# Kernel optimization log

Hardware: AMD Instinct MI355X
Metric: run time of the kernel (lower is better)

Reference implementation:

```python
import jax, jax.numpy as jnp
import numpy as np

B, T = 16384, 79
DIMS = [(1, 64), (64, 32), (32, 16), (16, 8), (8, 16), (16, 32), (32, 64), (64, 79)]


def _simple_rnn(x, Wx, Wh, b, act, return_seq):
    # x: [B, T, D] -> SimpleRNN: h_t = act(x_t @ Wx + h_{t-1} @ Wh + b)
    xb = jnp.einsum('btd,du->btu', x, Wx) + b  # precompute input projection
    h0 = jnp.zeros((x.shape[0], Wh.shape[0]), x.dtype)

    def step(h, xt):
        h = act(xt + h @ Wh)
        return h, h

    hT, hs = jax.lax.scan(step, h0, jnp.swapaxes(xb, 0, 1))  # scan over time
    return jnp.swapaxes(hs, 0, 1) if return_seq else hT


def setup_inputs() -> dict:
    key = jax.random.key(0)
    ks = jax.random.split(key, 3 * len(DIMS) + 1)
    inp = {"x": jax.random.normal(ks[0], (B, T), dtype=jnp.float32)}
    for i, (d, u) in enumerate(DIMS):
        inp[f"Wx{i}"] = jax.random.normal(ks[1 + 3 * i], (d, u), dtype=jnp.float32) / np.sqrt(d).astype(np.float32)
        inp[f"Wh{i}"] = jax.random.normal(ks[2 + 3 * i], (u, u), dtype=jnp.float32) / np.sqrt(u).astype(np.float32)
        inp[f"b{i}"] = jnp.zeros((u,), dtype=jnp.float32)
    return inp


def reference(x, Wx0, Wh0, b0, Wx1, Wh1, b1, Wx2, Wh2, b2, Wx3, Wh3, b3,
              Wx4, Wh4, b4, Wx5, Wh5, b5, Wx6, Wh6, b6, Wx7, Wh7, b7):
    params = [(Wx0, Wh0, b0), (Wx1, Wh1, b1), (Wx2, Wh2, b2), (Wx3, Wh3, b3),
              (Wx4, Wh4, b4), (Wx5, Wh5, b5), (Wx6, Wh6, b6), (Wx7, Wh7, b7)]
    h = x[..., None]  # [B, T, 1]  (tf.expand_dims(x, -1))
    n = len(params)
    for i, (Wx, Wh, b) in enumerate(params):
        last = i == n - 1
        act = jax.nn.sigmoid if last else jax.nn.relu
        h = _simple_rnn(h, Wx, Wh, b, act, return_seq=not last)
    return h  # decoded: [B, 79]
```

## Files before the change

kernel.cpp:

```cpp
#include <hip/hip_runtime.h>
#include <hip/hip_bf16.h>

#define DEVFN static __device__ __forceinline__

typedef short bf16x8 __attribute__((ext_vector_type(8)));
typedef float f32x4  __attribute__((ext_vector_type(4)));

constexpr int TSEQ  = 79;
constexpr int MWG   = 16;
constexpr int ROWU  = 344;
constexpr int NBLK  = 16384 / 64;

constexpr int LD[8]   = {1,64,32,16,8,16,32,64};
constexpr int LU[8]   = {64,32,16,8,16,32,64,79};
constexpr int LS[8]   = {0,8,72,104,120,128,144,176};
constexpr int LO[8]   = {8,72,104,120,128,144,176,240};
constexpr int LKP[8]  = {96,96,64,32,32,64,96,160};
constexpr int LKS[8]  = {3,3,2,1,1,2,3,5};
constexpr int LUP[8]  = {64,32,16,16,16,32,64,80};
constexpr int WOFF[8] = {0,6144,9216,10240,10752,11264,13312,19456};
constexpr int WTOTAL  = 32256;

constexpr int NT[8]  = {4,2,1,1,1,2,4,5};
constexpr int AO[8]  = {0,12,18,20,21,22,26,38};
constexpr int TO[8]  = {0,4,6,7,8,9,11,15};
constexpr int NH[8]  = {3,1,1,0,0,1,2,3};
constexpr int BHO[8] = {0,3,4,5,5,5,6,8};
constexpr int KORD[8][5] = {
  {0,1,2,0,0},{2,0,1,0,0},{1,0,0,0,0},{0,0,0,0,0},
  {0,0,0,0,0},{1,0,0,0,0},{1,2,0,0,0},{2,3,4,0,1}};

DEVFN unsigned short f2bf(float f) {
  unsigned int u = __builtin_bit_cast(unsigned int, f);
  return (unsigned short)((u + 0x7FFFu + ((u >> 16) & 1u)) >> 16);
}
DEVFN unsigned int pk_rna(float a, float b) {
  unsigned int ua = __builtin_bit_cast(unsigned int, a) + 0x8000u;
  unsigned int ub = __builtin_bit_cast(unsigned int, b) + 0x8000u;
  return __builtin_amdgcn_perm(ub, ua, 0x07060302u);
}
DEVFN float sigmoidf(float v) {
  return __builtin_amdgcn_rcpf(1.0f + __expf(-v));
}

__global__ void __launch_bounds__(256) prep_weights(
    const float* Wx0, const float* Wh0, const float* Wx1, const float* Wh1,
    const float* Wx2, const float* Wh2, const float* Wx3, const float* Wh3,
    const float* Wx4, const float* Wh4, const float* Wx5, const float* Wh5,
    const float* Wx6, const float* Wh6, const float* Wx7, const float* Wh7,
    unsigned short* __restrict__ wt)
{
  const float* wxp[8] = {Wx0,Wx1,Wx2,Wx3,Wx4,Wx5,Wx6,Wx7};
  const float* whp[8] = {Wh0,Wh1,Wh2,Wh3,Wh4,Wh5,Wh6,Wh7};
  int idx = blockIdx.x * 256 + threadIdx.x;
  if (idx >= WTOTAL) return;
#pragma unroll
  for (int l = 0; l < 8; ++l) {
    int sz = LUP[l] * LKP[l];
    if (idx >= WOFF[l] && idx < WOFF[l] + sz) {
      int local = idx - WOFF[l];
      int j = local / LKP[l];
      int k = local - j * LKP[l];
      float v = 0.f;
      if (j < LU[l]) {
        if (l == 0) {
          if (k == 0) v = Wx0[j];
          else if (k >= 8 && k < 72) v = Wh0[(k - 8) * 64 + j];
        } else {
          if (k < LD[l]) v = wxp[l][k * LU[l] + j];
          else if (k < LD[l] + LU[l]) v = whp[l][(k - LD[l]) * LU[l] + j];
        }
      }
      wt[idx] = f2bf(v);
    }
  }
}

DEVFN void preload_all(const unsigned short* __restrict__ wt,
                       const float* const (&bptr)[8], int lane,
                       bf16x8 (&af)[63], f32x4 (&bi)[20])
{
  const int m0 = lane & 15, quad = lane >> 4;
#pragma unroll
  for (int l = 0; l < 8; ++l) {
#pragma unroll
    for (int t = 0; t < 5; ++t) {
      if (t >= NT[l]) continue;
      const unsigned short* base = wt + WOFF[l] + (t * 16 + m0) * LKP[l];
#pragma unroll
      for (int k = 0; k < 5; ++k) {
        if (k >= LKS[l]) continue;
        af[AO[l] + t * LKS[l] + k] =
            *reinterpret_cast<const bf16x8*>(base + k * 32 + quad * 8);
      }
      const float* bp = bptr[l];
      f32x4 bv;
#pragma unroll
      for (int r = 0; r < 4; ++r) {
        int j2 = t * 16 + quad * 4 + r;
        bv[r] = (j2 < LU[l]) ? bp[j2] : 0.0f;
      }
      bi[TO[l] + t] = bv;
    }
  }
}

template <int L, bool LAST>
DEVFN void layer(const unsigned short* rbase,
                 unsigned short* wbase,
                 const bf16x8 (&af)[63], const f32x4 (&bi)[20],
                 const bf16x8 (&bh)[11],
                 float* __restrict__ out, int bb, int m, int quad)
{
  constexpr int ks = LKS[L], nt = NT[L], S = LS[L], O = LO[L], u = LU[L];
  bf16x8 fr[5];
#pragma unroll
  for (int i = 0; i < 5; ++i) {
    if (i < NH[L] || i >= ks) continue;
    fr[i] = *reinterpret_cast<const bf16x8*>(rbase + S + KORD[L][i] * 32);
  }
  f32x4 acc[5];
#pragma unroll
  for (int i = 0; i < 5; ++i) {
    if (i >= ks) continue;
    bf16x8 b = (i < NH[L]) ? bh[BHO[L] + i] : fr[i];
#pragma unroll
    for (int t = 0; t < 5; ++t) {
      if (t >= nt) continue;
      acc[t] = __builtin_amdgcn_mfma_f32_16x16x32_bf16(
          af[AO[L] + t * ks + KORD[L][i]], b,
          (i == 0) ? bi[TO[L] + t] : acc[t], 0, 0, 0);
    }
  }
#pragma unroll
  for (int t = 0; t < 5; ++t) {
    if (t >= nt) continue;
    const int jb = t * 16 + quad * 4;
    float v0 = acc[t][0], v1 = acc[t][1], v2 = acc[t][2], v3 = acc[t][3];
    if (L == 7) {
      v0 = sigmoidf(v0); v1 = sigmoidf(v1); v2 = sigmoidf(v2); v3 = sigmoidf(v3);
      if (LAST) {
        float* op = out + (size_t)(bb + m) * 79 + jb;
        if (jb + 0 < 79) op[0] = v0;
        if (jb + 1 < 79) op[1] = v1;
        if (jb + 2 < 79) op[2] = v2;
        if (jb + 3 < 79) op[3] = v3;
      } else {
        uint2 pk;
        pk.x = pk_rna(v0, v1);
        pk.y = pk_rna(v2, v3);
        *reinterpret_cast<uint2*>(wbase + O + t * 16) = pk;
      }
    } else {
      if (jb < u) {
        v0 = fmaxf(v0, 0.f); v1 = fmaxf(v1, 0.f); v2 = fmaxf(v2, 0.f); v3 = fmaxf(v3, 0.f);
        uint2 pk;
        pk.x = pk_rna(v0, v1);
        pk.y = pk_rna(v2, v3);
        *reinterpret_cast<uint2*>(wbase + O + t * 16) = pk;
      }
    }
  }
}

template <bool LAST>
DEVFN void timestep(int t, unsigned short (&hw)[MWG][ROWU],
                    const unsigned short (&xw)[MWG][80],
                    const bf16x8 (&af)[63], const f32x4 (&bi)[20],
                    float* __restrict__ out, int bb, int lane)
{
  const int m = lane & 15, quad = lane >> 4;
  const unsigned short* rbase = &hw[m][quad * 8];
  unsigned short* wbase = &hw[m][quad * 4];
  if (lane < MWG) hw[lane][0] = xw[lane][t];
  bf16x8 bh[11];
#pragma unroll
  for (int l = 0; l < 8; ++l) {
#pragma unroll
    for (int i = 0; i < 3; ++i) {
      if (i >= NH[l]) continue;
      bh[BHO[l] + i] =
          *reinterpret_cast<const bf16x8*>(rbase + LS[l] + KORD[l][i] * 32);
    }
  }
  layer<0, LAST>(rbase, wbase, af, bi, bh, out, bb, m, quad);
  layer<1, LAST>(rbase, wbase, af, bi, bh, out, bb, m, quad);
  layer<2, LAST>(rbase, wbase, af, bi, bh, out, bb, m, quad);
  layer<3, LAST>(rbase, wbase, af, bi, bh, out, bb, m, quad);
  layer<4, LAST>(rbase, wbase, af, bi, bh, out, bb, m, quad);
  layer<5, LAST>(rbase, wbase, af, bi, bh, out, bb, m, quad);
  layer<6, LAST>(rbase, wbase, af, bi, bh, out, bb, m, quad);
  layer<7, LAST>(rbase, wbase, af, bi, bh, out, bb, m, quad);
}

__global__ void __launch_bounds__(256)
__attribute__((amdgpu_waves_per_eu(1, 1)))
rnn_reg(const float* __restrict__ x, const unsigned short* __restrict__ wt,
        const float* b0, const float* b1, const float* b2, const float* b3,
        const float* b4, const float* b5, const float* b6, const float* b7,
        float* __restrict__ out)
{
  __shared__ __align__(16) unsigned short hb[4][MWG][ROWU];
  __shared__ __align__(4)  unsigned short xl[4][MWG][80];
  const int tid = threadIdx.x, lane = tid & 63, wid = tid >> 6;
  const int bb = blockIdx.x * 64 + wid * MWG;
  const float* bptr[8] = {b0, b1, b2, b3, b4, b5, b6, b7};

  {
    unsigned int* p = (unsigned int*)&hb[0][0][0];
    constexpr int NW = 4 * MWG * ROWU / 2;
    for (int i = tid; i < NW; i += 256) p[i] = 0;
  }
  {
    const float* xb = x + (size_t)blockIdx.x * 64 * TSEQ;
    for (int i = tid; i < 64 * TSEQ; i += 256) {
      int r = i / TSEQ, c = i - r * TSEQ;
      xl[r >> 4][r & 15][c] = f2bf(xb[i]);
    }
  }
  bf16x8 af[63];
  f32x4  bi[20];
  preload_all(wt, bptr, lane, af, bi);
  __syncthreads();

  unsigned short (&hw)[MWG][ROWU] = hb[wid];
  const unsigned short (&xw)[MWG][80] = xl[wid];

#pragma unroll 1
  for (int t = 0; t < TSEQ - 1; ++t)
    timestep<false>(t, hw, xw, af, bi, out, bb, lane);
  timestep<true>(TSEQ - 1, hw, xw, af, bi, out, bb, lane);
}

extern "C" void kernel_launch(void* const* d_in, const int* in_sizes, int n_in,
                              void* d_out, int out_size, void* d_ws, size_t ws_size,
                              hipStream_t stream)
{
  const float* x = (const float*)d_in[0];
  const float* Wx[8]; const float* Wh[8]; const float* b[8];
  for (int i = 0; i < 8; ++i) {
    Wx[i] = (const float*)d_in[1 + 3 * i];
    Wh[i] = (const float*)d_in[2 + 3 * i];
    b[i]  = (const float*)d_in[3 + 3 * i];
  }
  unsigned short* wt = (unsigned short*)d_ws;

  prep_weights<<<(WTOTAL + 255) / 256, 256, 0, stream>>>(
      Wx[0], Wh[0], Wx[1], Wh[1], Wx[2], Wh[2], Wx[3], Wh[3],
      Wx[4], Wh[4], Wx[5], Wh[5], Wx[6], Wh[6], Wx[7], Wh[7], wt);

  rnn_reg<<<NBLK, 256, 0, stream>>>(
      x, wt, b[0], b[1], b[2], b[3], b[4], b[5], b[6], b[7], (float*)d_out);
}
```

Before: 243.3 us.

## Skew layer recurrence into wavefront schedule with double-buffered LDS hidden state

Layers are now processed on a diagonal wavefront: at global step s, layer L handles time s-L. Each step reads from one LDS buffer and writes to the other, so the eight layers within a step no longer depend on each other. The goal is to break the serial layer-to-layer dependency chain (MFMA then LDS round trip) within each timestep and let MFMAs from different layers overlap. The cost is 7 extra fill/drain steps, a second LDS state buffer, and per-layer runtime guards that may limit how well the compiler interleaves work across layers. It also drops the hoisted early loads of the recurrent operands.

```diff
diff --git a/kernel.cpp b/kernel.cpp
--- a/kernel.cpp
+++ b/kernel.cpp
@@ -7,6 +7,7 @@
 typedef float f32x4  __attribute__((ext_vector_type(4)));
 
 constexpr int TSEQ  = 79;
+constexpr int NSTEP = TSEQ + 7;
 constexpr int MWG   = 16;
 constexpr int ROWU  = 344;
 constexpr int NBLK  = 16384 / 64;
@@ -24,11 +25,6 @@
 constexpr int NT[8]  = {4,2,1,1,1,2,4,5};
 constexpr int AO[8]  = {0,12,18,20,21,22,26,38};
 constexpr int TO[8]  = {0,4,6,7,8,9,11,15};
-constexpr int NH[8]  = {3,1,1,0,0,1,2,3};
-constexpr int BHO[8] = {0,3,4,5,5,5,6,8};
-constexpr int KORD[8][5] = {
-  {0,1,2,0,0},{2,0,1,0,0},{1,0,0,0,0},{0,0,0,0,0},
-  {0,0,0,0,0},{1,0,0,0,0},{1,2,0,0,0},{2,3,4,0,1}};
 
 DEVFN unsigned short f2bf(float f) {
   unsigned int u = __builtin_bit_cast(unsigned int, f);
@@ -106,31 +102,22 @@
 }
 
 template <int L, bool LAST>
-DEVFN void layer(const unsigned short* rbase,
-                 unsigned short* wbase,
-                 const bf16x8 (&af)[63], const f32x4 (&bi)[20],
-                 const bf16x8 (&bh)[11],
-                 float* __restrict__ out, int bb, int m, int quad)
+DEVFN void layerW(int s, const unsigned short* rbase, unsigned short* wbase,
+                  const bf16x8 (&af)[63], const f32x4 (&bi)[20],
+                  float* __restrict__ out, int bb, int m, int quad)
 {
   constexpr int ks = LKS[L], nt = NT[L], S = LS[L], O = LO[L], u = LU[L];
-  bf16x8 fr[5];
-#pragma unroll
-  for (int i = 0; i < 5; ++i) {
-    if (i < NH[L] || i >= ks) continue;
-    fr[i] = *reinterpret_cast<const bf16x8*>(rbase + S + KORD[L][i] * 32);
-  }
+  if (s < L || s > L + TSEQ - 1) return;
   f32x4 acc[5];
 #pragma unroll
-  for (int i = 0; i < 5; ++i) {
-    if (i >= ks) continue;
-    bf16x8 b = (i < NH[L]) ? bh[BHO[L] + i] : fr[i];
-#pragma unroll
-    for (int t = 0; t < 5; ++t) {
-      if (t >= nt) continue;
-      acc[t] = __builtin_amdgcn_mfma_f32_16x16x32_bf16(
-          af[AO[L] + t * ks + KORD[L][i]], b,
-          (i == 0) ? bi[TO[L] + t] : acc[t], 0, 0, 0);
-    }
+  for (int k = 0; k < 5; ++k) {
+    if (k >= ks) continue;
+    bf16x8 b = *reinterpret_cast<const bf16x8*>(rbase + S + k * 32);
+#pragma unroll
+    for (int t = 0; t < 5; ++t)
+      if (t < nt)
+        acc[t] = __builtin_amdgcn_mfma_f32_16x16x32_bf16(
+            af[AO[L] + t * ks + k], b, (k == 0) ? bi[TO[L] + t] : acc[t], 0, 0, 0);
   }
 #pragma unroll
   for (int t = 0; t < 5; ++t) {
@@ -164,33 +151,23 @@
 }
 
 template <bool LAST>
-DEVFN void timestep(int t, unsigned short (&hw)[MWG][ROWU],
-                    const unsigned short (&xw)[MWG][80],
-                    const bf16x8 (&af)[63], const f32x4 (&bi)[20],
-                    float* __restrict__ out, int bb, int lane)
+DEVFN void stepW(int s, unsigned short (&rb)[MWG][ROWU], unsigned short (&wb)[MWG][ROWU],
+                 const unsigned short (&xw)[MWG][80],
+                 const bf16x8 (&af)[63], const f32x4 (&bi)[20],
+                 float* __restrict__ out, int bb, int lane)
 {
   const int m = lane & 15, quad = lane >> 4;
-  const unsigned short* rbase = &hw[m][quad * 8];
-  unsigned short* wbase = &hw[m][quad * 4];
-  if (lane < MWG) hw[lane][0] = xw[lane][t];
-  bf16x8 bh[11];
-#pragma unroll
-  for (int l = 0; l < 8; ++l) {
-#pragma unroll
-    for (int i = 0; i < 3; ++i) {
-      if (i >= NH[l]) continue;
-      bh[BHO[l] + i] =
-          *reinterpret_cast<const bf16x8*>(rbase + LS[l] + KORD[l][i] * 32);
-    }
-  }
-  layer<0, LAST>(rbase, wbase, af, bi, bh, out, bb, m, quad);
-  layer<1, LAST>(rbase, wbase, af, bi, bh, out, bb, m, quad);
-  layer<2, LAST>(rbase, wbase, af, bi, bh, out, bb, m, quad);
-  layer<3, LAST>(rbase, wbase, af, bi, bh, out, bb, m, quad);
-  layer<4, LAST>(rbase, wbase, af, bi, bh, out, bb, m, quad);
-  layer<5, LAST>(rbase, wbase, af, bi, bh, out, bb, m, quad);
-  layer<6, LAST>(rbase, wbase, af, bi, bh, out, bb, m, quad);
-  layer<7, LAST>(rbase, wbase, af, bi, bh, out, bb, m, quad);
+  if (lane < MWG && s < TSEQ) rb[lane][0] = xw[lane][s];
+  const unsigned short* rbase = &rb[m][quad * 8];
+  unsigned short* wbase = &wb[m][quad * 4];
+  layerW<0, LAST>(s, rbase, wbase, af, bi, out, bb, m, quad);
+  layerW<1, LAST>(s, rbase, wbase, af, bi, out, bb, m, quad);
+  layerW<2, LAST>(s, rbase, wbase, af, bi, out, bb, m, quad);
+  layerW<3, LAST>(s, rbase, wbase, af, bi, out, bb, m, quad);
+  layerW<4, LAST>(s, rbase, wbase, af, bi, out, bb, m, quad);
+  layerW<5, LAST>(s, rbase, wbase, af, bi, out, bb, m, quad);
+  layerW<6, LAST>(s, rbase, wbase, af, bi, out, bb, m, quad);
+  layerW<7, LAST>(s, rbase, wbase, af, bi, out, bb, m, quad);
 }
 
 __global__ void __launch_bounds__(256)
@@ -200,16 +177,18 @@
         const float* b4, const float* b5, const float* b6, const float* b7,
         float* __restrict__ out)
 {
-  __shared__ __align__(16) unsigned short hb[4][MWG][ROWU];
+  __shared__ __align__(16) unsigned short hb0[4][MWG][ROWU];
+  __shared__ __align__(16) unsigned short hb1[4][MWG][ROWU];
   __shared__ __align__(4)  unsigned short xl[4][MWG][80];
   const int tid = threadIdx.x, lane = tid & 63, wid = tid >> 6;
   const int bb = blockIdx.x * 64 + wid * MWG;
   const float* bptr[8] = {b0, b1, b2, b3, b4, b5, b6, b7};
 
   {
-    unsigned int* p = (unsigned int*)&hb[0][0][0];
+    unsigned int* p0 = (unsigned int*)&hb0[0][0][0];
+    unsigned int* p1 = (unsigned int*)&hb1[0][0][0];
     constexpr int NW = 4 * MWG * ROWU / 2;
-    for (int i = tid; i < NW; i += 256) p[i] = 0;
+    for (int i = tid; i < NW; i += 256) { p0[i] = 0; p1[i] = 0; }
   }
   {
     const float* xb = x + (size_t)blockIdx.x * 64 * TSEQ;
@@ -223,13 +202,17 @@
   preload_all(wt, bptr, lane, af, bi);
   __syncthreads();
 
-  unsigned short (&hw)[MWG][ROWU] = hb[wid];
+  unsigned short (&hw0)[MWG][ROWU] = hb0[wid];
+  unsigned short (&hw1)[MWG][ROWU] = hb1[wid];
   const unsigned short (&xw)[MWG][80] = xl[wid];
 
 #pragma unroll 1
-  for (int t = 0; t < TSEQ - 1; ++t)
-    timestep<false>(t, hw, xw, af, bi, out, bb, lane);
-  timestep<true>(TSEQ - 1, hw, xw, af, bi, out, bb, lane);
+  for (int s = 0; s < NSTEP - 2; s += 2) {
+    stepW<false>(s,     hw0, hw1, xw, af, bi, out, bb, lane);
+    stepW<false>(s + 1, hw1, hw0, xw, af, bi, out, bb, lane);
+  }
+  stepW<false>(NSTEP - 2, hw0, hw1, xw, af, bi, out, bb, lane);
+  stepW<true >(NSTEP - 1, hw1, hw0, xw, af, bi, out, bb, lane);
 }
 
 extern "C" void kernel_launch(void* const* d_in, const int* in_sizes, int n_in,
```

Result: slower. 272.7 us (+12.1%).
